# Optimization experiments

Measured on AMD Instinct MI355X. Metric: run time of the kernel, lower is better.

## Reference

```python
import jax, jax.numpy as jnp
import numpy as np
from math import factorial, sqrt, pi

RS_IN = [(16, 0, 0), (16, 1, 0), (16, 2, 0)]
RS_OUT = [(16, 0, 0), (16, 1, 0), (16, 2, 0)]
HIDDEN = 100

def _l_filters(l_in, l_out):
    return list(range(abs(l_in - l_out), l_in + l_out + 1))

SET_L = sorted({l for _, li, _ in RS_IN for _, lo, _ in RS_OUT for l in _l_filters(li, lo)})
N_IN = sum(m * (2 * l + 1) for m, l, _ in RS_IN)
N_OUT = sum(m * (2 * l + 1) for m, l, _ in RS_OUT)
N_PATH = sum(mo * mi * len(_l_filters(li, lo)) for mo, lo, _ in RS_OUT for mi, li, _ in RS_IN)

def _cg_complex(j1, j2, j3):
    # Racah formula for SU(2) Clebsch-Gordan <j1 m1 j2 m2 | j3 m3> (integer l)
    f = lambda n: float(factorial(n))
    C = np.zeros((2 * j1 + 1, 2 * j2 + 1, 2 * j3 + 1))
    pref0 = sqrt((2 * j3 + 1) * f(j1 + j2 - j3) * f(j1 - j2 + j3) * f(-j1 + j2 + j3) / f(j1 + j2 + j3 + 1))
    for m1 in range(-j1, j1 + 1):
        for m2 in range(-j2, j2 + 1):
            m3 = m1 + m2
            if abs(m3) > j3:
                continue
            pref = pref0 * sqrt(f(j3 + m3) * f(j3 - m3) * f(j1 - m1) * f(j1 + m1) * f(j2 - m2) * f(j2 + m2))
            klo = max(0, j2 - j3 - m1, j1 + m2 - j3)
            khi = min(j1 + j2 - j3, j1 - m1, j2 + m2)
            s = 0.0
            for k in range(klo, khi + 1):
                s += (-1) ** k / (f(k) * f(j1 + j2 - j3 - k) * f(j1 - m1 - k) * f(j2 + m2 - k) * f(j3 - j2 + m1 + k) * f(j3 - j1 - m2 + k))
            C[j1 + m1, j2 + m2, j3 + m3] = pref * s
    return C

def _w3j(j1, j2, j3):
    cg = _cg_complex(j1, j2, j3)
    W = np.zeros_like(cg)
    for m3 in range(-j3, j3 + 1):
        W[:, :, j3 + m3] = (-1) ** (j1 - j2 + m3) / sqrt(2 * j3 + 1) * cg[:, :, j3 - m3]
    return W

def _Q(l):
    # complex -> real spherical-harmonic change of basis, rows m_real=-l..l, cols m=-l..l
    q = np.zeros((2 * l + 1, 2 * l + 1), dtype=complex)
    q[l, l] = 1.0
    s2 = 1.0 / sqrt(2.0)
    for m in range(1, l + 1):
        q[l + m, l + m] = (-1) ** m * s2
        q[l + m, l - m] = s2
        q[l - m, l - m] = 1j * s2
        q[l - m, l + m] = -1j * (-1) ** m * s2
    return q

def _real_cg(l1, l2, l3):
    # rotation-invariant 3-tensor in the real irrep basis, unit Frobenius norm (e3nn convention)
    c = np.einsum('am,bn,ck,mnk->abc', _Q(l1), _Q(l2), _Q(l3), _w3j(l1, l2, l3).astype(complex))
    re, im = np.real(c), np.imag(c)
    c = re if np.linalg.norm(re) >= np.linalg.norm(im) else im
    return jnp.asarray((c / np.linalg.norm(c)).astype(np.float32))

_CG = {}
for _mo, _lo, _ in RS_OUT:
    for _mi, _li, _ in RS_IN:
        for _lf in _l_filters(_li, _lo):
            if (_lo, _li, _lf) not in _CG:
                _CG[(_lo, _li, _lf)] = _real_cg(_lo, _li, _lf)

def _norm_coef():
    nc = np.zeros((len(RS_OUT), len(RS_IN), 2), dtype=np.float32)
    for i, (mul_out, l_out, _) in enumerate(RS_OUT):
        num = sum(mi * len(_l_filters(li, l_out)) for mi, li, _ in RS_IN)
        for j, (mul_in, l_in, _) in enumerate(RS_IN):
            lm = sqrt(2 * l_in + 1) * sqrt(4 * pi)  # normalization='norm'
            nc[i, j, 0] = lm / sqrt(num)
            nc[i, j, 1] = lm / sqrt(mul_in)
    return jnp.asarray(nc)

NORM_COEF = _norm_coef()

def _sh(u):
    # u: [B,3] unit vectors -> [25,B] real orthonormal SH, l=0..4, m=-l..l
    x, y, z = u[:, 0], u[:, 1], u[:, 2]
    x2, y2, z2 = x * x, y * y, z * z
    ys = [
        jnp.full_like(x, 0.5 * sqrt(1 / pi)),
        sqrt(3 / (4 * pi)) * y, sqrt(3 / (4 * pi)) * z, sqrt(3 / (4 * pi)) * x,
        0.5 * sqrt(15 / pi) * x * y, 0.5 * sqrt(15 / pi) * y * z, 0.25 * sqrt(5 / pi) * (3 * z2 - 1),
        0.5 * sqrt(15 / pi) * x * z, 0.25 * sqrt(15 / pi) * (x2 - y2),
        0.25 * sqrt(35 / (2 * pi)) * y * (3 * x2 - y2), 0.5 * sqrt(105 / pi) * x * y * z,
        0.25 * sqrt(21 / (2 * pi)) * y * (5 * z2 - 1), 0.25 * sqrt(7 / pi) * z * (5 * z2 - 3),
        0.25 * sqrt(21 / (2 * pi)) * x * (5 * z2 - 1), 0.25 * sqrt(105 / pi) * (x2 - y2) * z,
        0.25 * sqrt(35 / (2 * pi)) * x * (x2 - 3 * y2),
        0.75 * sqrt(35 / pi) * x * y * (x2 - y2), 0.75 * sqrt(35 / (2 * pi)) * y * (3 * x2 - y2) * z,
        0.75 * sqrt(5 / pi) * x * y * (7 * z2 - 1), 0.75 * sqrt(5 / (2 * pi)) * y * z * (7 * z2 - 3),
        (3.0 / 16.0) * sqrt(1 / pi) * (35 * z2 * z2 - 30 * z2 + 3),
        0.75 * sqrt(5 / (2 * pi)) * x * z * (7 * z2 - 3), (3.0 / 8.0) * sqrt(5 / pi) * (x2 - y2) * (7 * z2 - 1),
        0.75 * sqrt(35 / (2 * pi)) * x * (x2 - 3 * y2) * z,
        (3.0 / 16.0) * sqrt(35 / pi) * (x2 * x2 - 6 * x2 * y2 + y2 * y2),
    ]
    return jnp.stack(ys, axis=0)

def _kernel_forward(r, W1, b1, W2):
    size = r.shape[:-1]
    r2 = r.reshape(-1, 3)
    radii = jnp.linalg.norm(r2, axis=1)                      # [B]
    u = r2 / jnp.maximum(radii, 1e-12)[:, None]
    Ys = _sh(u)                                              # [25, B]
    h = jax.nn.relu(radii[:, None] * W1[0] + b1)             # radial MLP: [B,H]
    coeff = h @ W2                                           # [B, N_PATH]
    is_zero = radii == 0
    begin_c = 0
    rows = []
    for i, (mul_out, l_out, _) in enumerate(RS_OUT):
        row = []
        for j, (mul_in, l_in, _) in enumerate(RS_IN):
            lfs = _l_filters(l_in, l_out)
            n = mul_out * mul_in * len(lfs)
            c = coeff[:, begin_c:begin_c + n].reshape(-1, mul_out, mul_in, len(lfs))
            begin_c += n
            K = 0
            for k, lf in enumerate(lfs):
                off = sum(2 * l + 1 for l in SET_L if l < lf)
                Y = Ys[off:off + 2 * lf + 1]                 # [2lf+1, B]
                C = _CG[(l_out, l_in, lf)]                   # [2lo+1, 2li+1, 2lf+1]
                K = K + jnp.einsum('ijk,kz,zuv->zuivj', C, Y, c[..., k])
            norm = jnp.where(is_zero, NORM_COEF[i, j, 1], NORM_COEF[i, j, 0])
            K = K * norm[:, None, None, None, None]
            row.append(K.reshape(-1, mul_out * (2 * l_out + 1), mul_in * (2 * l_in + 1)))
        rows.append(jnp.concatenate(row, axis=2))
    kernel = jnp.concatenate(rows, axis=1)                   # [B, N_OUT, N_IN]
    return kernel.reshape(*size, N_OUT, N_IN)

def setup_inputs() -> dict:
    key = jax.random.key(0)
    k1, k2, k3, k4 = jax.random.split(key, 4)
    B = 8192
    return {
        'r': jax.random.normal(k1, (B, 3), dtype=jnp.float32),
        'W1': jax.random.normal(k2, (1, HIDDEN), dtype=jnp.float32),
        'b1': jax.random.normal(k3, (HIDDEN,), dtype=jnp.float32) * 0.1,
        'W2': jax.random.normal(k4, (HIDDEN, N_PATH), dtype=jnp.float32) / sqrt(HIDDEN),
    }

def reference(r, W1, b1, W2):
    return _kernel_forward(r, W1, b1, W2)
```

## Files before the change

kernel.cpp:

```cpp
#include <hip/hip_runtime.h>

#define NB     8192
#define NPB    4
#define NPATH  4864
#define NHID   100
#define NROW   144
#define NYSH   25
#define NDPAD  312

__device__ __align__(16) unsigned short g_w2r[NHID * 256 * 24];
__device__ float g_cg[1225];

__device__ inline double dfact(int n) {
    const double F[13] = {1., 1., 2., 6., 24., 120., 720., 5040., 40320.,
                          362880., 3628800., 39916800., 479001600.};
    return F[n];
}

__device__ double cgc(int j1, int j2, int j3, int m1, int m2, int m3) {
    if (m1 + m2 != m3) return 0.0;
    double pref0 = sqrt((2 * j3 + 1) * dfact(j1 + j2 - j3) * dfact(j1 - j2 + j3) *
                        dfact(-j1 + j2 + j3) / dfact(j1 + j2 + j3 + 1));
    double pref = pref0 * sqrt(dfact(j3 + m3) * dfact(j3 - m3) * dfact(j1 - m1) *
                               dfact(j1 + m1) * dfact(j2 - m2) * dfact(j2 + m2));
    int klo = max(0, max(j2 - j3 - m1, j1 + m2 - j3));
    int khi = min(j1 + j2 - j3, min(j1 - m1, j2 + m2));
    double s = 0.0;
    for (int k = klo; k <= khi; k++) {
        double d = dfact(k) * dfact(j1 + j2 - j3 - k) * dfact(j1 - m1 - k) *
                   dfact(j2 + m2 - k) * dfact(j3 - j2 + m1 + k) * dfact(j3 - j1 - m2 + k);
        s += ((k & 1) ? -1.0 : 1.0) / d;
    }
    return pref * s;
}

__device__ double w3jf(int j1, int j2, int j3, int m1, int m2, int m3) {
    int e = j1 - j2 + m3;
    double sgn = (e & 1) ? -1.0 : 1.0;
    return sgn / sqrt((double)(2 * j3 + 1)) * cgc(j1, j2, j3, m1, m2, -m3);
}

__device__ int qrow(int l, int a, int* col, double* re, double* im) {
    const double s2 = 0.70710678118654752440;
    int m = a - l;
    if (m == 0) { col[0] = l; re[0] = 1.0; im[0] = 0.0; return 1; }
    if (m > 0) {
        col[0] = l + m; re[0] = (m & 1) ? -s2 : s2; im[0] = 0.0;
        col[1] = l - m; re[1] = s2;                 im[1] = 0.0;
        return 2;
    }
    int mm = -m;
    col[0] = l - mm; re[0] = 0.0; im[0] = s2;
    col[1] = l + mm; re[1] = 0.0; im[1] = (mm & 1) ? s2 : -s2;
    return 2;
}

__global__ void setup_kernel(const float* __restrict__ W2) {
    const int tid = threadIdx.x;
    const int bid = blockIdx.x;
    if (bid >= 19) {
        int idx = (bid - 19) * 256 + tid;
        if (idx < NHID * 256 * 19) {
            const int CBJ[19]  = {0, 256, 512, 768, 1024, 1024, 1024, 1792, 1792, 1792,
                                  2560, 2816, 2816, 2816, 3584, 3584, 3584, 3584, 3584};
            const int NLFJ[19] = {1, 1, 1, 1, 3, 3, 3, 3, 3, 3, 1, 3, 3, 3, 5, 5, 5, 5, 5};
            const int KJ[19]   = {0, 0, 0, 0, 0, 1, 2, 0, 1, 2, 0, 0, 1, 2, 0, 1, 2, 3, 4};
            int j = idx % 19;
            int t = (idx / 19) & 255;
            int i = idx / (19 * 256);
            int p = CBJ[j] + t * NLFJ[j] + KJ[j];
            unsigned int u = __float_as_uint(W2[i * NPATH + p]);
            unsigned int rr = (u + 0x7fffu + ((u >> 16) & 1u)) >> 16;
            g_w2r[(i * 256 + t) * 24 + j] = (unsigned short)rr;
        }
        return;
    }
    const int TLO[19]  = {0,0,0,1,1,1,1,1,1,1,2,2,2,2,2,2,2,2,2};
    const int TLI[19]  = {0,1,2,0,1,1,1,2,2,2,0,1,1,1,2,2,2,2,2};
    const int TLF[19]  = {0,1,2,1,0,1,2,1,2,3,2,1,2,3,0,1,2,3,4};
    const int TOFF[19] = {0,1,10,35,44,53,80,125,170,245,350,375,420,495,600,625,700,825,1000};
    const int lo = TLO[bid], li = TLI[bid], lf = TLF[bid];
    const int n1 = 2 * lo + 1, n2 = 2 * li + 1, n3 = 2 * lf + 1;
    const int E = n1 * n2 * n3;

    __shared__ double sre[256], sim[256];
    __shared__ double snorm;
    __shared__ int ssel;

    double vre = 0.0, vim = 0.0;
    if (tid < E) {
        int g = tid % n3; int ab = tid / n3; int b = ab % n2; int a = ab / n2;
        int ca[2], cb[2], cc[2];
        double ra[2], ia[2], rb[2], ib[2], rc[2], ic[2];
        int na = qrow(lo, a, ca, ra, ia);
        int nb = qrow(li, b, cb, rb, ib);
        int nc = qrow(lf, g, cc, rc, ic);
        for (int p = 0; p < na; p++)
            for (int q = 0; q < nb; q++) {
                double pr = ra[p] * rb[q] - ia[p] * ib[q];
                double pi = ra[p] * ib[q] + ia[p] * rb[q];
                for (int s = 0; s < nc; s++) {
                    double w = w3jf(lo, li, lf, ca[p] - lo, cb[q] - li, cc[s] - lf);
                    if (w == 0.0) continue;
                    vre += (pr * rc[s] - pi * ic[s]) * w;
                    vim += (pr * ic[s] + pi * rc[s]) * w;
                }
            }
    }
    sre[tid] = vre * vre;
    sim[tid] = vim * vim;
    __syncthreads();
    if (tid == 0) {
        double sr = 0.0, si = 0.0;
        for (int e = 0; e < E; e++) { sr += sre[e]; si += sim[e]; }
        sr = sqrt(sr); si = sqrt(si);
        ssel = (sr >= si) ? 0 : 1;
        snorm = ssel ? si : sr;
    }
    __syncthreads();
    if (tid < E) {
        double val = ssel ? vim : vre;
        g_cg[TOFF[bid] + tid] = (float)(val / snorm);
    }
}


template <int LO, int LI, int CIDX, int PB, int RB, int CO, int NUM>
__device__ __forceinline__ void expand_small(const float* __restrict__ A,
                                             const float* __restrict__ D,
                                             float* __restrict__ op,
                                             int u, int v, bool zero) {
    constexpr int NO = 2 * LO + 1, NI = 2 * LI + 1, T = NO * NI;
    const float PI4 = 12.566370614359172f;
    const float n0 = sqrtf((2 * LI + 1) * PI4 / (float)NUM);
    const float n1 = sqrtf((2 * LI + 1) * PI4) * 0.25f;
    const float c0 = (zero ? n1 : n0) * A[CIDX];
    float rb[8];
    float4 t0 = *(const float4*)(D + PB);
    rb[0] = t0.x; rb[1] = t0.y; rb[2] = t0.z; rb[3] = t0.w;
    if constexpr (T > 4) rb[4] = D[PB + 4];
    float* o = op + (RB + u * NO) * NROW + CO + v * NI;
#pragma unroll
    for (int io = 0; io < NO; io++)
#pragma unroll
        for (int jo = 0; jo < NI; jo++)
            o[io * NROW + jo] = c0 * rb[io * NI + jo];
}

template <int LO, int LI, int NLF, int CIDX, int PB, int PST, int RB, int CO, int NUM>
__device__ __forceinline__ void expand_big(const float* __restrict__ A,
                                           const float* __restrict__ D,
                                           float* __restrict__ op,
                                           int u, int v, bool zero) {
    constexpr int NO = 2 * LO + 1, NI = 2 * LI + 1;
    constexpr int CH = (NI * NLF + 3) / 4;
    const float PI4 = 12.566370614359172f;
    const float n0 = sqrtf((2 * LI + 1) * PI4 / (float)NUM);
    const float n1 = sqrtf((2 * LI + 1) * PI4) * 0.25f;
    const float norm = zero ? n1 : n0;
    float c[NLF];
#pragma unroll
    for (int k = 0; k < NLF; k++) c[k] = norm * A[CIDX + k];
    float* o = op + (RB + u * NO) * NROW + CO + v * NI;
#pragma unroll
    for (int io = 0; io < NO; io++) {
        const float4* dp = (const float4*)(D + PB + io * PST);
        float rb[CH * 4];
#pragma unroll
        for (int q = 0; q < CH; q++) {
            float4 t = dp[q];
            rb[4 * q] = t.x; rb[4 * q + 1] = t.y; rb[4 * q + 2] = t.z; rb[4 * q + 3] = t.w;
        }
#pragma unroll
        for (int jo = 0; jo < NI; jo++) {
            float s = 0.0f;
#pragma unroll
            for (int k = 0; k < NLF; k++) s += rb[jo * NLF + k] * c[k];
            o[io * NROW + jo] = s;
        }
    }
}

#define BF16LO(x) __uint_as_float((x) << 16)
#define BF16HI(x) __uint_as_float((x) & 0xffff0000u)

__global__ __launch_bounds__(256, 4) void tfn_kernel(const float* __restrict__ r,
                                                     const float* __restrict__ W1,
                                                     const float* __restrict__ b1,
                                                     float* __restrict__ out) {
    __shared__ float sY[NPB][NYSH];
    __shared__ float sD[NPB][NDPAD];
    __shared__ float sRad[NPB];
    __shared__ int   sZero[NPB];

    const int tid = threadIdx.x;
    const int zbase = blockIdx.x * NPB;

    if (tid < NPB) {
        int z = zbase + tid;
        float* Y = sY[tid];
        float x = r[3 * z], y = r[3 * z + 1], zc = r[3 * z + 2];
        float rad = sqrtf(x * x + y * y + zc * zc);
        sRad[tid] = rad;
        sZero[tid] = (rad == 0.0f) ? 1 : 0;
        float inv = 1.0f / fmaxf(rad, 1e-12f);
        x *= inv; y *= inv; zc *= inv;
        float x2 = x * x, y2 = y * y, z2 = zc * zc;
        Y[0] = 0.28209479177387814f;
        Y[1] = 0.4886025119029199f * y;
        Y[2] = 0.4886025119029199f * zc;
        Y[3] = 0.4886025119029199f * x;
        Y[4] = 1.0925484305920792f * x * y;
        Y[5] = 1.0925484305920792f * y * zc;
        Y[6] = 0.31539156525252005f * (3.0f * z2 - 1.0f);
        Y[7] = 1.0925484305920792f * x * zc;
        Y[8] = 0.5462742152960396f * (x2 - y2);
        Y[9]  = 0.5900435899266435f * y * (3.0f * x2 - y2);
        Y[10] = 2.890611442640554f * x * y * zc;
        Y[11] = 0.4570457994644658f * y * (5.0f * z2 - 1.0f);
        Y[12] = 0.3731763325901154f * zc * (5.0f * z2 - 3.0f);
        Y[13] = 0.4570457994644658f * x * (5.0f * z2 - 1.0f);
        Y[14] = 1.445305721320277f * (x2 - y2) * zc;
        Y[15] = 0.5900435899266435f * x * (x2 - 3.0f * y2);
        Y[16] = 2.5033429417967046f * x * y * (x2 - y2);
        Y[17] = 1.7701307697799304f * y * (3.0f * x2 - y2) * zc;
        Y[18] = 0.9461746957575601f * x * y * (7.0f * z2 - 1.0f);
        Y[19] = 0.6690465435572892f * y * zc * (7.0f * z2 - 3.0f);
        Y[20] = 0.10578554691520431f * (35.0f * z2 * z2 - 30.0f * z2 + 3.0f);
        Y[21] = 0.6690465435572892f * x * zc * (7.0f * z2 - 3.0f);
        Y[22] = 0.47308734787878004f * (x2 - y2) * (7.0f * z2 - 1.0f);
        Y[23] = 1.7701307697799304f * x * (x2 - 3.0f * y2) * zc;
        Y[24] = 0.6258357354491761f * (x2 * x2 - 6.0f * x2 * y2 + y2 * y2);
    }
    __syncthreads();

    {
        const int dbase[10] = {0, 1, 4, 9, 12, 39, 84, 89, 134, 259};
        const int pnlf[9]   = {1, 1, 1, 1, 3, 3, 1, 3, 5};
        const int plf0[9]   = {0, 1, 2, 1, 0, 1, 2, 1, 0};
        const int ptab0[9]  = {0, 1, 2, 3, 4, 7, 10, 11, 14};
        const int toff[19]  = {0,1,10,35,44,53,80,125,170,245,350,375,420,495,600,625,700,825,1000};
        const int PBt[9]  = {0, 4, 8, 16, 20, 56, 104, 112, 172};
        const int PSTt[9] = {0, 0, 0, 0, 12, 16, 0, 12, 28};
        const int NIt[9]  = {1, 3, 5, 1, 3, 5, 1, 3, 5};
        for (int idx = tid; idx < NPB * 259; idx += 256) {
            int zz = idx / 259, e = idx - zz * 259;
            int pp = 8;
            while (e < dbase[pp]) pp--;
            int le = e - dbase[pp];
            int nlf = pnlf[pp];
            int rr = le / nlf, k = le - rr * nlf;
            int lf = plf0[pp] + k, nf = 2 * lf + 1;
            const float* cg = &g_cg[toff[ptab0[pp] + k] + rr * nf];
            const float* Yp = &sY[zz][lf * lf];
            float s = 0.0f;
            for (int m = 0; m < nf; m++) s += cg[m] * Yp[m];
            int pa;
            if (PSTt[pp] == 0) {
                pa = PBt[pp] + le;
            } else {
                int io = rr / NIt[pp];
                int jo = rr - io * NIt[pp];
                pa = PBt[pp] + io * PSTt[pp] + jo * nlf + k;
            }
            sD[zz][pa] = s;
        }
    }

    float rad0 = sRad[0], rad1 = sRad[1], rad2 = sRad[2], rad3 = sRad[3];
    float acc[NPB][19];
#pragma unroll
    for (int zz = 0; zz < NPB; zz++)
#pragma unroll
        for (int j = 0; j < 19; j++) acc[zz][j] = 0.0f;
    {
        const unsigned int* wp = (const unsigned int*)g_w2r + tid * 12;
        for (int i = 0; i < NHID; i++) {
            uint4 a  = *(const uint4*)(wp);
            uint4 b  = *(const uint4*)(wp + 4);
            uint2 c2 = *(const uint2*)(wp + 8);
            wp += 256 * 12;
            float w1i = W1[i], b1i = b1[i];
            float h0 = fmaxf(rad0 * w1i + b1i, 0.0f);
            float h1 = fmaxf(rad1 * w1i + b1i, 0.0f);
            float h2 = fmaxf(rad2 * w1i + b1i, 0.0f);
            float h3 = fmaxf(rad3 * w1i + b1i, 0.0f);
            float w[19];
            w[0]  = BF16LO(a.x);  w[1]  = BF16HI(a.x);
            w[2]  = BF16LO(a.y);  w[3]  = BF16HI(a.y);
            w[4]  = BF16LO(a.z);  w[5]  = BF16HI(a.z);
            w[6]  = BF16LO(a.w);  w[7]  = BF16HI(a.w);
            w[8]  = BF16LO(b.x);  w[9]  = BF16HI(b.x);
            w[10] = BF16LO(b.y);  w[11] = BF16HI(b.y);
            w[12] = BF16LO(b.z);  w[13] = BF16HI(b.z);
            w[14] = BF16LO(b.w);  w[15] = BF16HI(b.w);
            w[16] = BF16LO(c2.x); w[17] = BF16HI(c2.x);
            w[18] = BF16LO(c2.y);
#pragma unroll
            for (int j = 0; j < 19; j++) {
                acc[0][j] += h0 * w[j];
                acc[1][j] += h1 * w[j];
                acc[2][j] += h2 * w[j];
                acc[3][j] += h3 * w[j];
            }
        }
    }
    __syncthreads();

    const int u = tid >> 4, v = tid & 15;
    int zf0 = sZero[0], zf1 = sZero[1], zf2 = sZero[2], zf3 = sZero[3];
#pragma unroll
    for (int zz = 0; zz < NPB; zz++) {
        float* op = out + (size_t)(zbase + zz) * (NROW * NROW);
        bool zero = (zz == 0 ? zf0 : zz == 1 ? zf1 : zz == 2 ? zf2 : zf3) != 0;
        const float* D = sD[zz];
        const float* A = acc[zz];
        expand_small<0, 0,        0,  0,       0,  0,  48 >(A, D, op, u, v, zero);
        expand_small<0, 1,        1,  4,       0, 16,  48 >(A, D, op, u, v, zero);
        expand_small<0, 2,        2,  8,       0, 64,  48 >(A, D, op, u, v, zero);
        expand_small<1, 0,        3, 16,      16,  0, 112 >(A, D, op, u, v, zero);
        expand_big < 1, 1, 3,    4, 20, 12,   16, 16, 112 >(A, D, op, u, v, zero);
        expand_big < 1, 2, 3,    7, 56, 16,   16, 64, 112 >(A, D, op, u, v, zero);
        expand_small<2, 0,       10, 104,     64,  0, 144 >(A, D, op, u, v, zero);
        expand_big < 2, 1, 3,   11, 112, 12,  64, 16, 144 >(A, D, op, u, v, zero);
        expand_big < 2, 2, 5,   14, 172, 28,  64, 64, 144 >(A, D, op, u, v, zero);
    }
}

extern "C" void kernel_launch(void* const* d_in, const int* in_sizes, int n_in,
                              void* d_out, int out_size, void* d_ws, size_t ws_size,
                              hipStream_t stream) {
    const float* r  = (const float*)d_in[0];
    const float* W1 = (const float*)d_in[1];
    const float* b1 = (const float*)d_in[2];
    const float* W2 = (const float*)d_in[3];
    float* out = (float*)d_out;

    setup_kernel<<<19 + (NHID * 256 * 19 + 255) / 256, 256, 0, stream>>>(W2);

    const int nblocks = NB / NPB;
    tfn_kernel<<<nblocks, 256, 0, stream>>>(r, W1, b1, out);
}
```

Baseline: 805.6 us.

## Split hidden-layer GEMM into two passes to cut accumulator register pressure

Splits the 19-coefficient per-thread accumulation into two passes: 10 coefficients for output rows l_out<=1, then 9 for l_out=2. Each pass is followed right away by its own output expansion. The bf16 weight table is re-laid out with padding so each pass reads one aligned 16-byte load plus one word. The aim is fewer live registers at 4 blocks per CU, so spilling or occupancy limits ease. The cost is looping over the hidden dimension twice, which re-issues the W1/b1 loads and ReLU work.

```diff
diff --git a/kernel.cpp b/kernel.cpp
--- a/kernel.cpp
+++ b/kernel.cpp
@@ -69,9 +69,10 @@
             int t = (idx / 19) & 255;
             int i = idx / (19 * 256);
             int p = CBJ[j] + t * NLFJ[j] + KJ[j];
+            int slot = (j < 10) ? j : (j + 2);
             unsigned int u = __float_as_uint(W2[i * NPATH + p]);
             unsigned int rr = (u + 0x7fffu + ((u >> 16) & 1u)) >> 16;
-            g_w2r[(i * 256 + t) * 24 + j] = (unsigned short)rr;
+            g_w2r[(i * 256 + t) * 24 + slot] = (unsigned short)rr;
         }
         return;
     }
@@ -124,9 +125,47 @@
     }
 }
 
-
-template <int LO, int LI, int CIDX, int PB, int RB, int CO, int NUM>
-__device__ __forceinline__ void expand_small(const float* __restrict__ A,
+#define BF16LO(x) __uint_as_float((x) << 16)
+#define BF16HI(x) __uint_as_float((x) & 0xffff0000u)
+
+template <int NP, int GOFF>
+__device__ __forceinline__ void gemm_pass(float (&acc)[NPB][NP], int tid,
+                                          const float* __restrict__ W1,
+                                          const float* __restrict__ b1,
+                                          float rad0, float rad1, float rad2,
+                                          float rad3) {
+#pragma unroll
+    for (int zz = 0; zz < NPB; zz++)
+#pragma unroll
+        for (int j = 0; j < NP; j++) acc[zz][j] = 0.0f;
+    const unsigned int* wp = (const unsigned int*)g_w2r + tid * 12 + GOFF;
+    for (int i = 0; i < NHID; i++) {
+        uint4 a = *(const uint4*)wp;
+        unsigned int e = wp[4];
+        wp += 256 * 12;
+        float w1i = W1[i], b1i = b1[i];
+        float h0 = fmaxf(rad0 * w1i + b1i, 0.0f);
+        float h1 = fmaxf(rad1 * w1i + b1i, 0.0f);
+        float h2 = fmaxf(rad2 * w1i + b1i, 0.0f);
+        float h3 = fmaxf(rad3 * w1i + b1i, 0.0f);
+        float w[NP];
+        unsigned int d[5] = {a.x, a.y, a.z, a.w, e};
+#pragma unroll
+        for (int j = 0; j < NP; j++)
+            w[j] = (j & 1) ? BF16HI(d[j >> 1]) : BF16LO(d[j >> 1]);
+#pragma unroll
+        for (int j = 0; j < NP; j++) {
+            acc[0][j] += h0 * w[j];
+            acc[1][j] += h1 * w[j];
+            acc[2][j] += h2 * w[j];
+            acc[3][j] += h3 * w[j];
+        }
+    }
+}
+
+
+template <int LO, int LI, int CIDX, int PB, int RB, int CO, int NUM, int NA>
+__device__ __forceinline__ void expand_small(const float (&A)[NA],
                                              const float* __restrict__ D,
                                              float* __restrict__ op,
                                              int u, int v, bool zero) {
@@ -147,8 +186,9 @@
             o[io * NROW + jo] = c0 * rb[io * NI + jo];
 }
 
-template <int LO, int LI, int NLF, int CIDX, int PB, int PST, int RB, int CO, int NUM>
-__device__ __forceinline__ void expand_big(const float* __restrict__ A,
+template <int LO, int LI, int NLF, int CIDX, int PB, int PST, int RB, int CO,
+          int NUM, int NA>
+__device__ __forceinline__ void expand_big(const float (&A)[NA],
                                            const float* __restrict__ D,
                                            float* __restrict__ op,
                                            int u, int v, bool zero) {
@@ -180,9 +220,6 @@
         }
     }
 }
-
-#define BF16LO(x) __uint_as_float((x) << 16)
-#define BF16HI(x) __uint_as_float((x) & 0xffff0000u)
 
 __global__ __launch_bounds__(256, 4) void tfn_kernel(const float* __restrict__ r,
                                                      const float* __restrict__ W1,
@@ -268,62 +305,40 @@
     }
 
     float rad0 = sRad[0], rad1 = sRad[1], rad2 = sRad[2], rad3 = sRad[3];
-    float acc[NPB][19];
-#pragma unroll
-    for (int zz = 0; zz < NPB; zz++)
-#pragma unroll
-        for (int j = 0; j < 19; j++) acc[zz][j] = 0.0f;
+    const int u = tid >> 4, v = tid & 15;
+
     {
-        const unsigned int* wp = (const unsigned int*)g_w2r + tid * 12;
-        for (int i = 0; i < NHID; i++) {
-            uint4 a  = *(const uint4*)(wp);
-            uint4 b  = *(const uint4*)(wp + 4);
-            uint2 c2 = *(const uint2*)(wp + 8);
-            wp += 256 * 12;
-            float w1i = W1[i], b1i = b1[i];
-            float h0 = fmaxf(rad0 * w1i + b1i, 0.0f);
-            float h1 = fmaxf(rad1 * w1i + b1i, 0.0f);
-            float h2 = fmaxf(rad2 * w1i + b1i, 0.0f);
-            float h3 = fmaxf(rad3 * w1i + b1i, 0.0f);
-            float w[19];
-            w[0]  = BF16LO(a.x);  w[1]  = BF16HI(a.x);
-            w[2]  = BF16LO(a.y);  w[3]  = BF16HI(a.y);
-            w[4]  = BF16LO(a.z);  w[5]  = BF16HI(a.z);
-            w[6]  = BF16LO(a.w);  w[7]  = BF16HI(a.w);
-            w[8]  = BF16LO(b.x);  w[9]  = BF16HI(b.x);
-            w[10] = BF16LO(b.y);  w[11] = BF16HI(b.y);
-            w[12] = BF16LO(b.z);  w[13] = BF16HI(b.z);
-            w[14] = BF16LO(b.w);  w[15] = BF16HI(b.w);
-            w[16] = BF16LO(c2.x); w[17] = BF16HI(c2.x);
-            w[18] = BF16LO(c2.y);
-#pragma unroll
-            for (int j = 0; j < 19; j++) {
-                acc[0][j] += h0 * w[j];
-                acc[1][j] += h1 * w[j];
-                acc[2][j] += h2 * w[j];
-                acc[3][j] += h3 * w[j];
-            }
-        }
-    }
-    __syncthreads();
-
-    const int u = tid >> 4, v = tid & 15;
-    int zf0 = sZero[0], zf1 = sZero[1], zf2 = sZero[2], zf3 = sZero[3];
-#pragma unroll
-    for (int zz = 0; zz < NPB; zz++) {
-        float* op = out + (size_t)(zbase + zz) * (NROW * NROW);
-        bool zero = (zz == 0 ? zf0 : zz == 1 ? zf1 : zz == 2 ? zf2 : zf3) != 0;
-        const float* D = sD[zz];
-        const float* A = acc[zz];
-        expand_small<0, 0,        0,  0,       0,  0,  48 >(A, D, op, u, v, zero);
-        expand_small<0, 1,        1,  4,       0, 16,  48 >(A, D, op, u, v, zero);
-        expand_small<0, 2,        2,  8,       0, 64,  48 >(A, D, op, u, v, zero);
-        expand_small<1, 0,        3, 16,      16,  0, 112 >(A, D, op, u, v, zero);
-        expand_big < 1, 1, 3,    4, 20, 12,   16, 16, 112 >(A, D, op, u, v, zero);
-        expand_big < 1, 2, 3,    7, 56, 16,   16, 64, 112 >(A, D, op, u, v, zero);
-        expand_small<2, 0,       10, 104,     64,  0, 144 >(A, D, op, u, v, zero);
-        expand_big < 2, 1, 3,   11, 112, 12,  64, 16, 144 >(A, D, op, u, v, zero);
-        expand_big < 2, 2, 5,   14, 172, 28,  64, 64, 144 >(A, D, op, u, v, zero);
+        float acc[NPB][10];
+        gemm_pass<10, 0>(acc, tid, W1, b1, rad0, rad1, rad2, rad3);
+        __syncthreads();
+        int zf0 = sZero[0], zf1 = sZero[1], zf2 = sZero[2], zf3 = sZero[3];
+#pragma unroll
+        for (int zz = 0; zz < NPB; zz++) {
+            float* op = out + (size_t)(zbase + zz) * (NROW * NROW);
+            bool zero = (zz == 0 ? zf0 : zz == 1 ? zf1 : zz == 2 ? zf2 : zf3) != 0;
+            const float* D = sD[zz];
+            expand_small<0, 0,        0,  0,       0,  0,  48 >(acc[zz], D, op, u, v, zero);
+            expand_small<0, 1,        1,  4,       0, 16,  48 >(acc[zz], D, op, u, v, zero);
+            expand_small<0, 2,        2,  8,       0, 64,  48 >(acc[zz], D, op, u, v, zero);
+            expand_small<1, 0,        3, 16,      16,  0, 112 >(acc[zz], D, op, u, v, zero);
+            expand_big < 1, 1, 3,    4, 20, 12,   16, 16, 112 >(acc[zz], D, op, u, v, zero);
+            expand_big < 1, 2, 3,    7, 56, 16,   16, 64, 112 >(acc[zz], D, op, u, v, zero);
+        }
+    }
+
+    {
+        float acc[NPB][9];
+        gemm_pass<9, 6>(acc, tid, W1, b1, rad0, rad1, rad2, rad3);
+        int zf0 = sZero[0], zf1 = sZero[1], zf2 = sZero[2], zf3 = sZero[3];
+#pragma unroll
+        for (int zz = 0; zz < NPB; zz++) {
+            float* op = out + (size_t)(zbase + zz) * (NROW * NROW);
+            bool zero = (zz == 0 ? zf0 : zz == 1 ? zf1 : zz == 2 ? zf2 : zf3) != 0;
+            const float* D = sD[zz];
+            expand_small<2, 0,        0, 104,     64,  0, 144 >(acc[zz], D, op, u, v, zero);
+            expand_big < 2, 1, 3,    1, 112, 12,  64, 16, 144 >(acc[zz], D, op, u, v, zero);
+            expand_big < 2, 2, 5,    4, 172, 28,  64, 64, 144 >(acc[zz], D, op, u, v, zero);
+        }
     }
 }
 
```

Result: slower. 844.8 us (+4.9%).

## Stage output row bands in per-wave LDS slabs and flush with coalesced nontemporal stores

Applied to the files above, without the earlier changes.

Each wave now writes its expanded kernel blocks into a private LDS slab covering a contiguous band of output rows, then copies the band to global memory as float4 nontemporal stores. Before, threads wrote scattered strided scalar stores straight to global memory. The aim is coalesced, streaming writes of the large output. The change adds about 46 KB of LDS per block and lowers launch bounds occupancy from 4 to 3. It relies on wave-level ordering, using only compiler barriers and no __syncthreads between slab writes and reads.

```diff
diff --git a/kernel.cpp b/kernel.cpp
--- a/kernel.cpp
+++ b/kernel.cpp
@@ -7,6 +7,8 @@
 #define NROW   144
 #define NYSH   25
 #define NDPAD  312
+
+typedef float v4f __attribute__((ext_vector_type(4)));
 
 __device__ __align__(16) unsigned short g_w2r[NHID * 256 * 24];
 __device__ float g_cg[1225];
@@ -125,21 +127,19 @@
 }
 
 
-template <int LO, int LI, int CIDX, int PB, int RB, int CO, int NUM>
-__device__ __forceinline__ void expand_small(const float* __restrict__ A,
+template <int NO, int NI, int CIDX, int PB, int NUM, int NA>
+__device__ __forceinline__ void expand_small(const float (&A)[NA],
                                              const float* __restrict__ D,
-                                             float* __restrict__ op,
-                                             int u, int v, bool zero) {
-    constexpr int NO = 2 * LO + 1, NI = 2 * LI + 1, T = NO * NI;
+                                             float* o, bool zero) {
+    constexpr int T = NO * NI;
     const float PI4 = 12.566370614359172f;
-    const float n0 = sqrtf((2 * LI + 1) * PI4 / (float)NUM);
-    const float n1 = sqrtf((2 * LI + 1) * PI4) * 0.25f;
+    const float n0 = sqrtf(NI * PI4 / (float)NUM);
+    const float n1 = sqrtf(NI * PI4) * 0.25f;
     const float c0 = (zero ? n1 : n0) * A[CIDX];
     float rb[8];
     float4 t0 = *(const float4*)(D + PB);
     rb[0] = t0.x; rb[1] = t0.y; rb[2] = t0.z; rb[3] = t0.w;
     if constexpr (T > 4) rb[4] = D[PB + 4];
-    float* o = op + (RB + u * NO) * NROW + CO + v * NI;
 #pragma unroll
     for (int io = 0; io < NO; io++)
 #pragma unroll
@@ -147,21 +147,18 @@
             o[io * NROW + jo] = c0 * rb[io * NI + jo];
 }
 
-template <int LO, int LI, int NLF, int CIDX, int PB, int PST, int RB, int CO, int NUM>
-__device__ __forceinline__ void expand_big(const float* __restrict__ A,
+template <int NO, int NI, int NLF, int CIDX, int PB, int PST, int NUM, int NA>
+__device__ __forceinline__ void expand_big(const float (&A)[NA],
                                            const float* __restrict__ D,
-                                           float* __restrict__ op,
-                                           int u, int v, bool zero) {
-    constexpr int NO = 2 * LO + 1, NI = 2 * LI + 1;
+                                           float* o, bool zero) {
     constexpr int CH = (NI * NLF + 3) / 4;
     const float PI4 = 12.566370614359172f;
-    const float n0 = sqrtf((2 * LI + 1) * PI4 / (float)NUM);
-    const float n1 = sqrtf((2 * LI + 1) * PI4) * 0.25f;
+    const float n0 = sqrtf(NI * PI4 / (float)NUM);
+    const float n1 = sqrtf(NI * PI4) * 0.25f;
     const float norm = zero ? n1 : n0;
     float c[NLF];
 #pragma unroll
     for (int k = 0; k < NLF; k++) c[k] = norm * A[CIDX + k];
-    float* o = op + (RB + u * NO) * NROW + CO + v * NI;
 #pragma unroll
     for (int io = 0; io < NO; io++) {
         const float4* dp = (const float4*)(D + PB + io * PST);
@@ -181,15 +178,35 @@
     }
 }
 
+template <int NROWS>
+__device__ __forceinline__ void flush_band(const float* slabW, float* gdst,
+                                           int lane) {
+    constexpr int N4 = NROWS * NROW / 4;
+    const v4f* s4 = (const v4f*)slabW;
+    v4f* g4 = (v4f*)gdst;
+#pragma unroll
+    for (int c = 0; c < N4 / 64; c++) {
+        v4f t = s4[c * 64 + lane];
+        __builtin_nontemporal_store(t, &g4[c * 64 + lane]);
+    }
+    if constexpr (N4 % 64) {
+        if (lane < (N4 % 64)) {
+            v4f t = s4[(N4 / 64) * 64 + lane];
+            __builtin_nontemporal_store(t, &g4[(N4 / 64) * 64 + lane]);
+        }
+    }
+}
+
 #define BF16LO(x) __uint_as_float((x) << 16)
 #define BF16HI(x) __uint_as_float((x) & 0xffff0000u)
 
-__global__ __launch_bounds__(256, 4) void tfn_kernel(const float* __restrict__ r,
+__global__ __launch_bounds__(256, 3) void tfn_kernel(const float* __restrict__ r,
                                                      const float* __restrict__ W1,
                                                      const float* __restrict__ b1,
                                                      float* __restrict__ out) {
     __shared__ float sY[NPB][NYSH];
     __shared__ float sD[NPB][NDPAD];
+    __shared__ float sSlab[4][20 * NROW];
     __shared__ float sRad[NPB];
     __shared__ int   sZero[NPB];
 
@@ -307,23 +324,40 @@
     }
     __syncthreads();
 
-    const int u = tid >> 4, v = tid & 15;
+    const int w = tid >> 6;
+    const int lane = tid & 63;
+    const int uw = (tid >> 4) & 3;
+    const int v = tid & 15;
+    float* slabW = &sSlab[w][0];
     int zf0 = sZero[0], zf1 = sZero[1], zf2 = sZero[2], zf3 = sZero[3];
+
 #pragma unroll
     for (int zz = 0; zz < NPB; zz++) {
-        float* op = out + (size_t)(zbase + zz) * (NROW * NROW);
+        float* gbase = out + (size_t)(zbase + zz) * (NROW * NROW);
         bool zero = (zz == 0 ? zf0 : zz == 1 ? zf1 : zz == 2 ? zf2 : zf3) != 0;
         const float* D = sD[zz];
-        const float* A = acc[zz];
-        expand_small<0, 0,        0,  0,       0,  0,  48 >(A, D, op, u, v, zero);
-        expand_small<0, 1,        1,  4,       0, 16,  48 >(A, D, op, u, v, zero);
-        expand_small<0, 2,        2,  8,       0, 64,  48 >(A, D, op, u, v, zero);
-        expand_small<1, 0,        3, 16,      16,  0, 112 >(A, D, op, u, v, zero);
-        expand_big < 1, 1, 3,    4, 20, 12,   16, 16, 112 >(A, D, op, u, v, zero);
-        expand_big < 1, 2, 3,    7, 56, 16,   16, 64, 112 >(A, D, op, u, v, zero);
-        expand_small<2, 0,       10, 104,     64,  0, 144 >(A, D, op, u, v, zero);
-        expand_big < 2, 1, 3,   11, 112, 12,  64, 16, 144 >(A, D, op, u, v, zero);
-        expand_big < 2, 2, 5,   14, 172, 28,  64, 64, 144 >(A, D, op, u, v, zero);
+        const float (&A)[19] = acc[zz];
+
+        expand_small<1, 1,   0,  0,  48>(A, D, slabW + uw * NROW + 0 + v * 1, zero);
+        expand_small<1, 3,   1,  4,  48>(A, D, slabW + uw * NROW + 16 + v * 3, zero);
+        expand_small<1, 5,   2,  8,  48>(A, D, slabW + uw * NROW + 64 + v * 5, zero);
+        asm volatile("" ::: "memory");
+        flush_band<4>(slabW, gbase + (4 * w) * NROW, lane);
+        asm volatile("" ::: "memory");
+
+        expand_small<3, 1,   3, 16, 112>(A, D, slabW + uw * 3 * NROW + 0 + v * 1, zero);
+        expand_big <3, 3, 3,  4, 20, 12, 112>(A, D, slabW + uw * 3 * NROW + 16 + v * 3, zero);
+        expand_big <3, 5, 3,  7, 56, 16, 112>(A, D, slabW + uw * 3 * NROW + 64 + v * 5, zero);
+        asm volatile("" ::: "memory");
+        flush_band<12>(slabW, gbase + (16 + 12 * w) * NROW, lane);
+        asm volatile("" ::: "memory");
+
+        expand_small<5, 1,  10, 104, 144>(A, D, slabW + uw * 5 * NROW + 0 + v * 1, zero);
+        expand_big <5, 3, 3, 11, 112, 12, 144>(A, D, slabW + uw * 5 * NROW + 16 + v * 3, zero);
+        expand_big <5, 5, 5, 14, 172, 28, 144>(A, D, slabW + uw * 5 * NROW + 64 + v * 5, zero);
+        asm volatile("" ::: "memory");
+        flush_band<20>(slabW, gbase + (64 + 20 * w) * NROW, lane);
+        asm volatile("" ::: "memory");
     }
 }
 
```

After: 786.6 us. -2.4%, faster.
